# Kernel tuning notes

Measured on AMD Instinct MI355X. Metric: run time of the kernel, lower is better.

## Reference

```python
import jax, jax.numpy as jnp
import numpy as np

# Blade ordering for G(3,0,1): [1, e0, e1, e2, e3, e01, e02, e03, e12, e13, e23, e012, e013, e023, e123, e0123]
_GRADES = np.array([0, 1, 1, 1, 1, 2, 2, 2, 2, 2, 2, 3, 3, 3, 3, 4])
# e0-wedge map: blade without e0 -> e0 ^ blade (all signs +1 with this ordering)
_E0_MAP = {0: 1, 2: 5, 3: 6, 4: 7, 8: 11, 9: 12, 10: 13, 14: 15}


def _make_basis():
    """9 Pin(3,0,1)-equivariant linear maps on 16-dim multivectors: B[9,16,16]."""
    B = np.zeros((9, 16, 16), dtype=np.float32)
    for g in range(5):  # grade projections
        for i, gi in enumerate(_GRADES):
            if gi == g:
                B[g, i, i] = 1.0
    for g in range(4):  # e0-wedge per grade
        for src, dst in _E0_MAP.items():
            if _GRADES[src] == g:
                B[5 + g, dst, src] = 1.0
    return jnp.asarray(B)


def setup_inputs() -> dict:
    key = jax.random.key(0)
    ks = jax.random.split(key, 9)
    n_parent, stride = 65536, 2
    in_mv, out_mv, in_s, out_s = 32, 32, 64, 64
    n_child = n_parent * stride
    return {
        "x_mv": jax.random.normal(ks[0], (n_parent, in_mv, 16), jnp.float32),
        "x_s": jax.random.normal(ks[1], (n_parent, in_s), jnp.float32),
        "skip_mv": jax.random.normal(ks[2], (n_child, out_mv, 16), jnp.float32),
        "skip_s": jax.random.normal(ks[3], (n_child, out_s), jnp.float32),
        "w_mv": jax.random.normal(ks[4], (out_mv, in_mv, 9), jnp.float32) * 0.1,
        "w_s2mv": jax.random.normal(ks[5], (out_mv, in_s), jnp.float32) * 0.1,
        "w_mv2s": jax.random.normal(ks[6], (out_s, in_mv), jnp.float32) * 0.1,
        "w_s2s": jax.random.normal(ks[7], (out_s, in_s), jnp.float32) * 0.1,
        "b_s": jax.random.normal(ks[8], (out_s,), jnp.float32) * 0.1,
        "stride": stride,
    }


def reference(x_mv, x_s, skip_mv, skip_s, w_mv, w_s2mv, w_mv2s, w_s2s, b_s, stride):
    B = _make_basis()
    # Propagate parents to children (repeat_interleave along node dim)
    xp_mv = jnp.repeat(x_mv, stride, axis=0)   # [Nc, in_mv, 16]
    xp_s = jnp.repeat(x_s, stride, axis=0)     # [Nc, in_s]
    # EquiLinear: combine 9 basis maps with channel-mixing weights
    W = jnp.einsum('oib,bjk->oijk', w_mv, B)   # [out_mv, in_mv, 16, 16]
    out_mv = jnp.einsum('nik,oijk->noj', xp_mv, W)  # [Nc, out_mv, 16]
    # scalars -> scalar (grade-0) component of multivectors
    out_mv = out_mv.at[:, :, 0].add(xp_s @ w_s2mv.T)
    # mv scalar component + scalars -> output scalars
    out_s = xp_mv[:, :, 0] @ w_mv2s.T + xp_s @ w_s2s.T + b_s
    # Residual add onto skip connection (children features)
    return skip_mv + out_mv, skip_s + out_s
```

## Files before the change

kernel.cpp:

```cpp
#include <hip/hip_runtime.h>

typedef __attribute__((ext_vector_type(8))) short bf16x8;
typedef __attribute__((ext_vector_type(4))) float f32x4;

#define THR 256
#define PBLK 32

__device__ __forceinline__ unsigned int bf_rne(float f) {
    unsigned int u = __float_as_uint(f);
    u += 0x7fffu + ((u >> 16) & 1u);
    return u >> 16;
}

#define MFMA(A, B, C) __builtin_amdgcn_mfma_f32_16x16x32_bf16((A), (B), (C), 0, 0, 0)

#define XB(ti, j, pl, slot) ((ti) * 8320 + (j) * 520 + (pl) * 32 + (slot) * 8)

__global__ __launch_bounds__(THR) void equi_mfma(
    const float* __restrict__ x_mv,
    const float* __restrict__ x_s,
    const float* __restrict__ skip_mv,
    const float* __restrict__ skip_s,
    const float* __restrict__ w_mv,
    const float* __restrict__ w_s2mv,
    const float* __restrict__ w_mv2s,
    const float* __restrict__ w_s2s,
    const float* __restrict__ b_s,
    float* __restrict__ out_mv,
    float* __restrict__ out_s,
    int n_parent, int stride)
{
    __shared__ char smem[39296];
    unsigned short* xb  = (unsigned short*)smem;
    unsigned short* xsb = (unsigned short*)(smem + 33280);
    float* y  = (float*)smem;
    float* ys = (float*)smem + 8736;

    const int t  = threadIdx.x;
    const int p0 = blockIdx.x * PBLK;

    {
        const float4* xg = (const float4*)(x_mv + (size_t)p0 * 512);
        #pragma unroll
        for (int k = 0; k < 16; ++k) {
            int id = t + k * THR;
            float4 v = xg[id];
            int p  = id >> 7;
            int i  = (id >> 2) & 31;
            int jq = id & 3;
            int ti = p >> 4, pl = p & 15;
            int ig = i >> 3, ie = i & 7;
            int slot = ig ^ (pl & 3) ^ jq;
            int base = XB(ti, jq * 4, pl, slot) + ie;
            xb[base + 0 * 520] = (unsigned short)bf_rne(v.x);
            xb[base + 1 * 520] = (unsigned short)bf_rne(v.y);
            xb[base + 2 * 520] = (unsigned short)bf_rne(v.z);
            xb[base + 3 * 520] = (unsigned short)bf_rne(v.w);
        }
        const float4* xsg = (const float4*)(x_s + (size_t)p0 * 64);
        #pragma unroll
        for (int k = 0; k < 2; ++k) {
            int id = t + k * THR;
            float4 v = xsg[id];
            int p = id >> 4;
            int s0 = (id & 15) * 4;
            int ti = p >> 4, pl = p & 15;
            int sg = s0 >> 3, se0 = s0 & 7;
            int a = ((ti * 16 + pl) * 8 + (sg ^ (pl & 7))) * 8 + se0;
            xsb[a + 0] = (unsigned short)bf_rne(v.x);
            xsb[a + 1] = (unsigned short)bf_rne(v.y);
            xsb[a + 2] = (unsigned short)bf_rne(v.z);
            xsb[a + 3] = (unsigned short)bf_rne(v.w);
        }
    }

    const int lane = t & 63;
    const int wid  = t >> 6;
    const int h   = wid & 1;
    const int jh  = wid >> 1;
    const int col = lane & 15;
    const int g4  = lane >> 4;
    const int kb  = g4 * 8;

    bf16x8 Bg[3], Bw[2];
    #pragma unroll
    for (int gg = 0; gg < 3; ++gg) {
        int b = 2 * jh + gg;
        #pragma unroll
        for (int e = 0; e < 8; ++e)
            Bg[gg][e] = (short)bf_rne(w_mv[(h * 16 + col) * 288 + (kb + e) * 9 + b]);
    }
    #pragma unroll
    for (int ww = 0; ww < 2; ++ww) {
        int b = 5 + 2 * jh + ww;
        #pragma unroll
        for (int e = 0; e < 8; ++e)
            Bw[ww][e] = (short)bf_rne(w_mv[(h * 16 + col) * 288 + (kb + e) * 9 + b]);
    }
    bf16x8 Bm2s[2], Bs2mv[2], Bs2s[2][2];
    if (jh == 0) {
        #pragma unroll
        for (int c = 0; c < 2; ++c)
            #pragma unroll
            for (int e = 0; e < 8; ++e)
                Bm2s[c][e] = (short)bf_rne(w_mv2s[((2 * h + c) * 16 + col) * 32 + kb + e]);
        #pragma unroll
        for (int kk = 0; kk < 2; ++kk) {
            #pragma unroll
            for (int e = 0; e < 8; ++e)
                Bs2mv[kk][e] = (short)bf_rne(w_s2mv[(h * 16 + col) * 64 + kk * 32 + kb + e]);
            #pragma unroll
            for (int c = 0; c < 2; ++c)
                #pragma unroll
                for (int e = 0; e < 8; ++e)
                    Bs2s[kk][c][e] = (short)bf_rne(w_s2s[((2 * h + c) * 16 + col) * 64 + kk * 32 + kb + e]);
        }
    }

    __syncthreads();

    f32x4 cj[2][8];
    f32x4 cs[2][2];
    #pragma unroll
    for (int ti = 0; ti < 2; ++ti) {
        #pragma unroll
        for (int jj = 0; jj < 8; ++jj) cj[ti][jj] = (f32x4){0.f, 0.f, 0.f, 0.f};
        cs[ti][0] = (f32x4){0.f, 0.f, 0.f, 0.f};
        cs[ti][1] = (f32x4){0.f, 0.f, 0.f, 0.f};
    }
    const int prow = col;

    if (jh == 0) {
        #pragma unroll
        for (int ti = 0; ti < 2; ++ti) {
            bf16x8 A0;
            #pragma unroll
            for (int jj = 0; jj < 8; ++jj) {
                int slot = g4 ^ (prow & 3) ^ (jj >> 2);
                bf16x8 A = *(const bf16x8*)&xb[XB(ti, jj, prow, slot)];
                if (jj == 0)      cj[ti][0] = MFMA(A, Bg[0], cj[ti][0]);
                else if (jj < 5)  cj[ti][jj] = MFMA(A, Bg[1], cj[ti][jj]);
                else              cj[ti][jj] = MFMA(A, Bg[2], cj[ti][jj]);
                if (jj == 0) { cj[ti][1] = MFMA(A, Bw[0], cj[ti][1]); A0 = A; }
                else if (jj == 2) cj[ti][5] = MFMA(A, Bw[1], cj[ti][5]);
                else if (jj == 3) cj[ti][6] = MFMA(A, Bw[1], cj[ti][6]);
                else if (jj == 4) cj[ti][7] = MFMA(A, Bw[1], cj[ti][7]);
            }
            cs[ti][0] = MFMA(A0, Bm2s[0], cs[ti][0]);
            cs[ti][1] = MFMA(A0, Bm2s[1], cs[ti][1]);
            #pragma unroll
            for (int kk = 0; kk < 2; ++kk) {
                const unsigned short* sp = &xsb[((ti * 16 + prow) * 8 + ((kk * 4 + g4) ^ (prow & 7))) * 8];
                bf16x8 Axs = *(const bf16x8*)sp;
                cj[ti][0] = MFMA(Axs, Bs2mv[kk], cj[ti][0]);
                cs[ti][0] = MFMA(Axs, Bs2s[kk][0], cs[ti][0]);
                cs[ti][1] = MFMA(Axs, Bs2s[kk][1], cs[ti][1]);
            }
        }
    } else {
        #pragma unroll
        for (int ti = 0; ti < 2; ++ti) {
            #pragma unroll
            for (int jj = 0; jj < 8; ++jj) {
                int j = 8 + jj;
                int slot = g4 ^ (prow & 3) ^ (j >> 2);
                bf16x8 A = *(const bf16x8*)&xb[XB(ti, j, prow, slot)];
                if (jj < 3)       cj[ti][jj] = MFMA(A, Bg[0], cj[ti][jj]);
                else if (jj < 7)  cj[ti][jj] = MFMA(A, Bg[1], cj[ti][jj]);
                else              cj[ti][jj] = MFMA(A, Bg[2], cj[ti][jj]);
                if (jj == 0)      cj[ti][3] = MFMA(A, Bw[0], cj[ti][3]);
                else if (jj == 1) cj[ti][4] = MFMA(A, Bw[0], cj[ti][4]);
                else if (jj == 2) cj[ti][5] = MFMA(A, Bw[0], cj[ti][5]);
                else if (jj == 6) cj[ti][7] = MFMA(A, Bw[1], cj[ti][7]);
            }
        }
    }

    #pragma unroll
    for (int hf = 0; hf < 2; ++hf) {
        __syncthreads();
        #pragma unroll
        for (int jj = 0; jj < 8; ++jj) {
            int j = jh * 8 + jj;
            #pragma unroll
            for (int r = 0; r < 4; ++r) {
                int p = g4 * 4 + r;
                y[j * 546 + p * 34 + h * 16 + col] = cj[hf][jj][r];
            }
        }
        if (jh == 0) {
            #pragma unroll
            for (int c = 0; c < 2; ++c)
                #pragma unroll
                for (int r = 0; r < 4; ++r) {
                    int p = g4 * 4 + r;
                    ys[p * 68 + (2 * h + c) * 16 + col] = cs[hf][c][r];
                }
        }
        __syncthreads();

        const int cbase = (p0 + hf * 16) * stride;
        const float4* sk4 = (const float4*)skip_mv;
        float4* om4 = (float4*)out_mv;
        const float4* sks4 = (const float4*)skip_s;
        float4* os4 = (float4*)out_s;
        const float4* bs4 = (const float4*)b_s;

        if (stride == 2) {
            const int totmv = 16 * 2 * 128;
            for (int id = t; id < totmv; id += THR) {
                int child = id >> 7, rem = id & 127;
                int o = rem >> 2, q = rem & 3;
                int ph = child >> 1;
                float4 ad;
                ad.x = y[(q * 4 + 0) * 546 + ph * 34 + o];
                ad.y = y[(q * 4 + 1) * 546 + ph * 34 + o];
                ad.z = y[(q * 4 + 2) * 546 + ph * 34 + o];
                ad.w = y[(q * 4 + 3) * 546 + ph * 34 + o];
                size_t gi = (size_t)(cbase + child) * 128 + rem;
                float4 s = sk4[gi];
                om4[gi] = make_float4(s.x + ad.x, s.y + ad.y, s.z + ad.z, s.w + ad.w);
            }
            const int tots = 16 * 2 * 16;
            for (int id = t; id < tots; id += THR) {
                int child = id >> 4, ch4 = id & 15;
                int ph = child >> 1;
                float4 ad = *(const float4*)&ys[ph * 68 + ch4 * 4];
                float4 bb = bs4[ch4];
                size_t gi = (size_t)(cbase + child) * 16 + ch4;
                float4 s = sks4[gi];
                os4[gi] = make_float4(s.x + ad.x + bb.x, s.y + ad.y + bb.y,
                                      s.z + ad.z + bb.z, s.w + ad.w + bb.w);
            }
        } else {
            const int totmv = 16 * stride * 128;
            for (int id = t; id < totmv; id += THR) {
                int child = id >> 7, rem = id & 127;
                int o = rem >> 2, q = rem & 3;
                int ph = child / stride;
                float4 ad;
                ad.x = y[(q * 4 + 0) * 546 + ph * 34 + o];
                ad.y = y[(q * 4 + 1) * 546 + ph * 34 + o];
                ad.z = y[(q * 4 + 2) * 546 + ph * 34 + o];
                ad.w = y[(q * 4 + 3) * 546 + ph * 34 + o];
                size_t gi = (size_t)(cbase + child) * 128 + rem;
                float4 s = sk4[gi];
                om4[gi] = make_float4(s.x + ad.x, s.y + ad.y, s.z + ad.z, s.w + ad.w);
            }
            const int tots = 16 * stride * 16;
            for (int id = t; id < tots; id += THR) {
                int child = id >> 4, ch4 = id & 15;
                int ph = child / stride;
                float4 ad = *(const float4*)&ys[ph * 68 + ch4 * 4];
                float4 bb = bs4[ch4];
                size_t gi = (size_t)(cbase + child) * 16 + ch4;
                float4 s = sks4[gi];
                os4[gi] = make_float4(s.x + ad.x + bb.x, s.y + ad.y + bb.y,
                                      s.z + ad.z + bb.z, s.w + ad.w + bb.w);
            }
        }
    }
}

__global__ __launch_bounds__(256) void equi_tail(
    const float* __restrict__ x_mv, const float* __restrict__ x_s,
    const float* __restrict__ skip_mv, const float* __restrict__ skip_s,
    const float* __restrict__ w_mv, const float* __restrict__ w_s2mv,
    const float* __restrict__ w_mv2s, const float* __restrict__ w_s2s,
    const float* __restrict__ b_s,
    float* __restrict__ out_mv, float* __restrict__ out_s,
    int pstart, int n_parent, int stride)
{
    int idx = blockIdx.x * blockDim.x + threadIdx.x;
    int o = idx & 31, pr = idx >> 5;
    int p = pstart + pr;
    if (p >= n_parent) return;
    float a[16];
    #pragma unroll
    for (int j = 0; j < 16; ++j) a[j] = 0.f;
    float s0 = 0.f, s1 = 0.f;
    const float4* xg = (const float4*)(x_mv + (size_t)p * 512);
    for (int i = 0; i < 32; ++i) {
        float4 X0 = xg[i * 4 + 0], X1 = xg[i * 4 + 1], X2 = xg[i * 4 + 2], X3 = xg[i * 4 + 3];
        const float* wp = &w_mv[o * 288 + i * 9];
        float w0 = wp[0], w1 = wp[1], w2 = wp[2], w3 = wp[3], w4 = wp[4];
        float w5 = wp[5], w6 = wp[6], w7 = wp[7], w8 = wp[8];
        a[0] += X0.x * w0;  a[1] += X0.y * w1 + X0.x * w5;
        a[2] += X0.z * w1;  a[3] += X0.w * w1;  a[4] += X1.x * w1;
        a[5] += X1.y * w2 + X0.z * w6;  a[6] += X1.z * w2 + X0.w * w6;
        a[7] += X1.w * w2 + X1.x * w6;  a[8] += X2.x * w2;
        a[9] += X2.y * w2;  a[10] += X2.z * w2;
        a[11] += X2.w * w3 + X2.x * w7;  a[12] += X3.x * w3 + X2.y * w7;
        a[13] += X3.y * w3 + X2.z * w7;  a[14] += X3.z * w3;
        a[15] += X3.w * w4 + X3.z * w8;
        s0 += X0.x * w_mv2s[o * 32 + i];
        s1 += X0.x * w_mv2s[(o + 32) * 32 + i];
    }
    for (int sc = 0; sc < 64; ++sc) {
        float xv = x_s[(size_t)p * 64 + sc];
        a[0] += xv * w_s2mv[o * 64 + sc];
        s0 += xv * w_s2s[o * 64 + sc];
        s1 += xv * w_s2s[(o + 32) * 64 + sc];
    }
    s0 += b_s[o]; s1 += b_s[o + 32];
    for (int r = 0; r < stride; ++r) {
        size_t c = (size_t)p * stride + r;
        const float4* sk = (const float4*)(skip_mv + c * 512 + o * 16);
        float4* om = (float4*)(out_mv + c * 512 + o * 16);
        float4 k0 = sk[0], k1 = sk[1], k2 = sk[2], k3 = sk[3];
        om[0] = make_float4(k0.x + a[0],  k0.y + a[1],  k0.z + a[2],  k0.w + a[3]);
        om[1] = make_float4(k1.x + a[4],  k1.y + a[5],  k1.z + a[6],  k1.w + a[7]);
        om[2] = make_float4(k2.x + a[8],  k2.y + a[9],  k2.z + a[10], k2.w + a[11]);
        om[3] = make_float4(k3.x + a[12], k3.y + a[13], k3.z + a[14], k3.w + a[15]);
        out_s[c * 64 + o]      = skip_s[c * 64 + o] + s0;
        out_s[c * 64 + o + 32] = skip_s[c * 64 + o + 32] + s1;
    }
}

extern "C" void kernel_launch(void* const* d_in, const int* in_sizes, int n_in,
                              void* d_out, int out_size, void* d_ws, size_t ws_size,
                              hipStream_t stream) {
    const float* x_mv    = (const float*)d_in[0];
    const float* x_s     = (const float*)d_in[1];
    const float* skip_mv = (const float*)d_in[2];
    const float* skip_s  = (const float*)d_in[3];
    const float* w_mv    = (const float*)d_in[4];
    const float* w_s2mv  = (const float*)d_in[5];
    const float* w_mv2s  = (const float*)d_in[6];
    const float* w_s2s   = (const float*)d_in[7];
    const float* b_s     = (const float*)d_in[8];

    const int n_parent = in_sizes[0] / 512;
    const int n_child  = in_sizes[2] / 512;
    const int stride   = n_child / n_parent;

    float* out_mv = (float*)d_out;
    float* out_s  = out_mv + (size_t)n_child * 512;

    const int full = n_parent >> 5;
    const int rem  = n_parent & 31;
    if (full > 0)
        equi_mfma<<<full, THR, 0, stream>>>(
            x_mv, x_s, skip_mv, skip_s, w_mv, w_s2mv, w_mv2s, w_s2s, b_s,
            out_mv, out_s, n_parent, stride);
    if (rem > 0) {
        int thr = rem * 32;
        int blk = (thr + 255) / 256;
        equi_tail<<<blk, 256, 0, stream>>>(
            x_mv, x_s, skip_mv, skip_s, w_mv, w_s2mv, w_mv2s, w_s2s, b_s,
            out_mv, out_s, full * 32, n_parent, stride);
    }
}
```

Baseline: 165.9 us.

## Vectorize LDS staging of inputs and outputs with XOR-swizzled layouts

The input staging is reorganised so each thread gathers 8 consecutive i-values per blade component and writes them to shared memory as a single 16-byte bf16x8 store, instead of many scattered 2-byte stores. The output staging buffer y is relaid out as [parent][out][16 components] with an XOR-swizzled quad index, so results are written and read as float4 rather than scalar accesses. The ys buffer is moved to reuse the xsb region, which shrinks shared memory. Global reads of x_mv become strided per thread rather than fully coalesced, and the swizzle has to be correct to avoid bank conflicts and wrong indexing.

```diff
diff --git a/kernel.cpp b/kernel.cpp
--- a/kernel.cpp
+++ b/kernel.cpp
@@ -15,6 +15,8 @@
 #define MFMA(A, B, C) __builtin_amdgcn_mfma_f32_16x16x32_bf16((A), (B), (C), 0, 0, 0)
 
 #define XB(ti, j, pl, slot) ((ti) * 8320 + (j) * 520 + (pl) * 32 + (slot) * 8)
+#define YPS 520
+#define YSS 68
 
 __global__ __launch_bounds__(THR) void equi_mfma(
     const float* __restrict__ x_mv,
@@ -30,48 +32,52 @@
     float* __restrict__ out_s,
     int n_parent, int stride)
 {
-    __shared__ char smem[39296];
+    __shared__ char smem[37632];
     unsigned short* xb  = (unsigned short*)smem;
     unsigned short* xsb = (unsigned short*)(smem + 33280);
     float* y  = (float*)smem;
-    float* ys = (float*)smem + 8736;
+    float* ys = (float*)(smem + 33280);
 
     const int t  = threadIdx.x;
     const int p0 = blockIdx.x * PBLK;
 
     {
+        const int p   = t >> 3;
+        const int ig2 = (t >> 2) & 1;
+        const int jq  = t & 3;
+        const int ti  = p >> 4, pl = p & 15;
         const float4* xg = (const float4*)(x_mv + (size_t)p0 * 512);
-        #pragma unroll
-        for (int k = 0; k < 16; ++k) {
-            int id = t + k * THR;
-            float4 v = xg[id];
-            int p  = id >> 7;
-            int i  = (id >> 2) & 31;
-            int jq = id & 3;
-            int ti = p >> 4, pl = p & 15;
-            int ig = i >> 3, ie = i & 7;
-            int slot = ig ^ (pl & 3) ^ jq;
-            int base = XB(ti, jq * 4, pl, slot) + ie;
-            xb[base + 0 * 520] = (unsigned short)bf_rne(v.x);
-            xb[base + 1 * 520] = (unsigned short)bf_rne(v.y);
-            xb[base + 2 * 520] = (unsigned short)bf_rne(v.z);
-            xb[base + 3 * 520] = (unsigned short)bf_rne(v.w);
-        }
+        const int base = p * 128 + ig2 * 64 + jq;
+        bf16x8 acc[4][2];
+        #pragma unroll
+        for (int s = 0; s < 16; ++s) {
+            float4 v = xg[base + s * 4];
+            int igl = s >> 3, e = s & 7;
+            acc[0][igl][e] = (short)bf_rne(v.x);
+            acc[1][igl][e] = (short)bf_rne(v.y);
+            acc[2][igl][e] = (short)bf_rne(v.z);
+            acc[3][igl][e] = (short)bf_rne(v.w);
+        }
+        #pragma unroll
+        for (int jo = 0; jo < 4; ++jo)
+            #pragma unroll
+            for (int igl = 0; igl < 2; ++igl) {
+                int ig = ig2 * 2 + igl;
+                int slot = ig ^ (pl & 3) ^ jq;
+                *(bf16x8*)&xb[XB(ti, jq * 4 + jo, pl, slot)] = acc[jo][igl];
+            }
+        const int q = t & 7;
+        const int ps = t >> 3;
+        const int tis = ps >> 4, pls = ps & 15;
         const float4* xsg = (const float4*)(x_s + (size_t)p0 * 64);
-        #pragma unroll
-        for (int k = 0; k < 2; ++k) {
-            int id = t + k * THR;
-            float4 v = xsg[id];
-            int p = id >> 4;
-            int s0 = (id & 15) * 4;
-            int ti = p >> 4, pl = p & 15;
-            int sg = s0 >> 3, se0 = s0 & 7;
-            int a = ((ti * 16 + pl) * 8 + (sg ^ (pl & 7))) * 8 + se0;
-            xsb[a + 0] = (unsigned short)bf_rne(v.x);
-            xsb[a + 1] = (unsigned short)bf_rne(v.y);
-            xsb[a + 2] = (unsigned short)bf_rne(v.z);
-            xsb[a + 3] = (unsigned short)bf_rne(v.w);
-        }
+        float4 v0 = xsg[ps * 16 + q * 2 + 0];
+        float4 v1 = xsg[ps * 16 + q * 2 + 1];
+        bf16x8 sv;
+        sv[0] = (short)bf_rne(v0.x); sv[1] = (short)bf_rne(v0.y);
+        sv[2] = (short)bf_rne(v0.z); sv[3] = (short)bf_rne(v0.w);
+        sv[4] = (short)bf_rne(v1.x); sv[5] = (short)bf_rne(v1.y);
+        sv[6] = (short)bf_rne(v1.z); sv[7] = (short)bf_rne(v1.w);
+        *(bf16x8*)&xsb[((tis * 16 + pls) * 8 + (q ^ (pls & 7))) * 8] = sv;
     }
 
     const int lane = t & 63;
@@ -81,6 +87,7 @@
     const int col = lane & 15;
     const int g4  = lane >> 4;
     const int kb  = g4 * 8;
+    const int oo  = h * 16 + col;
 
     bf16x8 Bg[3], Bw[2];
     #pragma unroll
@@ -88,14 +95,14 @@
         int b = 2 * jh + gg;
         #pragma unroll
         for (int e = 0; e < 8; ++e)
-            Bg[gg][e] = (short)bf_rne(w_mv[(h * 16 + col) * 288 + (kb + e) * 9 + b]);
+            Bg[gg][e] = (short)bf_rne(w_mv[oo * 288 + (kb + e) * 9 + b]);
     }
     #pragma unroll
     for (int ww = 0; ww < 2; ++ww) {
         int b = 5 + 2 * jh + ww;
         #pragma unroll
         for (int e = 0; e < 8; ++e)
-            Bw[ww][e] = (short)bf_rne(w_mv[(h * 16 + col) * 288 + (kb + e) * 9 + b]);
+            Bw[ww][e] = (short)bf_rne(w_mv[oo * 288 + (kb + e) * 9 + b]);
     }
     bf16x8 Bm2s[2], Bs2mv[2], Bs2s[2][2];
     if (jh == 0) {
@@ -108,7 +115,7 @@
         for (int kk = 0; kk < 2; ++kk) {
             #pragma unroll
             for (int e = 0; e < 8; ++e)
-                Bs2mv[kk][e] = (short)bf_rne(w_s2mv[(h * 16 + col) * 64 + kk * 32 + kb + e]);
+                Bs2mv[kk][e] = (short)bf_rne(w_s2mv[oo * 64 + kk * 32 + kb + e]);
             #pragma unroll
             for (int c = 0; c < 2; ++c)
                 #pragma unroll
@@ -180,22 +187,26 @@
     for (int hf = 0; hf < 2; ++hf) {
         __syncthreads();
         #pragma unroll
-        for (int jj = 0; jj < 8; ++jj) {
-            int j = jh * 8 + jj;
-            #pragma unroll
-            for (int r = 0; r < 4; ++r) {
-                int p = g4 * 4 + r;
-                y[j * 546 + p * 34 + h * 16 + col] = cj[hf][jj][r];
+        for (int r = 0; r < 4; ++r) {
+            int p = g4 * 4 + r;
+            #pragma unroll
+            for (int q4 = 0; q4 < 2; ++q4) {
+                int jqg  = jh * 2 + q4;
+                int quad = jqg ^ (oo & 3) ^ g4;
+                float4 w;
+                w.x = cj[hf][q4 * 4 + 0][r];
+                w.y = cj[hf][q4 * 4 + 1][r];
+                w.z = cj[hf][q4 * 4 + 2][r];
+                w.w = cj[hf][q4 * 4 + 3][r];
+                *(float4*)&y[p * YPS + oo * 16 + quad * 4] = w;
             }
         }
         if (jh == 0) {
             #pragma unroll
             for (int c = 0; c < 2; ++c)
                 #pragma unroll
-                for (int r = 0; r < 4; ++r) {
-                    int p = g4 * 4 + r;
-                    ys[p * 68 + (2 * h + c) * 16 + col] = cs[hf][c][r];
-                }
+                for (int r = 0; r < 4; ++r)
+                    ys[(g4 * 4 + r) * YSS + (2 * h + c) * 16 + col] = cs[hf][c][r];
         }
         __syncthreads();
 
@@ -212,11 +223,8 @@
                 int child = id >> 7, rem = id & 127;
                 int o = rem >> 2, q = rem & 3;
                 int ph = child >> 1;
-                float4 ad;
-                ad.x = y[(q * 4 + 0) * 546 + ph * 34 + o];
-                ad.y = y[(q * 4 + 1) * 546 + ph * 34 + o];
-                ad.z = y[(q * 4 + 2) * 546 + ph * 34 + o];
-                ad.w = y[(q * 4 + 3) * 546 + ph * 34 + o];
+                int quad = q ^ (o & 3) ^ (ph >> 2);
+                float4 ad = *(const float4*)&y[ph * YPS + o * 16 + quad * 4];
                 size_t gi = (size_t)(cbase + child) * 128 + rem;
                 float4 s = sk4[gi];
                 om4[gi] = make_float4(s.x + ad.x, s.y + ad.y, s.z + ad.z, s.w + ad.w);
@@ -225,7 +233,7 @@
             for (int id = t; id < tots; id += THR) {
                 int child = id >> 4, ch4 = id & 15;
                 int ph = child >> 1;
-                float4 ad = *(const float4*)&ys[ph * 68 + ch4 * 4];
+                float4 ad = *(const float4*)&ys[ph * YSS + ch4 * 4];
                 float4 bb = bs4[ch4];
                 size_t gi = (size_t)(cbase + child) * 16 + ch4;
                 float4 s = sks4[gi];
@@ -238,11 +246,8 @@
                 int child = id >> 7, rem = id & 127;
                 int o = rem >> 2, q = rem & 3;
                 int ph = child / stride;
-                float4 ad;
-                ad.x = y[(q * 4 + 0) * 546 + ph * 34 + o];
-                ad.y = y[(q * 4 + 1) * 546 + ph * 34 + o];
-                ad.z = y[(q * 4 + 2) * 546 + ph * 34 + o];
-                ad.w = y[(q * 4 + 3) * 546 + ph * 34 + o];
+                int quad = q ^ (o & 3) ^ (ph >> 2);
+                float4 ad = *(const float4*)&y[ph * YPS + o * 16 + quad * 4];
                 size_t gi = (size_t)(cbase + child) * 128 + rem;
                 float4 s = sk4[gi];
                 om4[gi] = make_float4(s.x + ad.x, s.y + ad.y, s.z + ad.z, s.w + ad.w);
@@ -251,7 +256,7 @@
             for (int id = t; id < tots; id += THR) {
                 int child = id >> 4, ch4 = id & 15;
                 int ph = child / stride;
-                float4 ad = *(const float4*)&ys[ph * 68 + ch4 * 4];
+                float4 ad = *(const float4*)&ys[ph * YSS + ch4 * 4];
                 float4 bb = bs4[ch4];
                 size_t gi = (size_t)(cbase + child) * 16 + ch4;
                 float4 s = sks4[gi];
```

New measurement: 163.5 us. Within noise of the previous version (-1.4%).
